# Kernel optimization log

Measured on AMD Instinct MI355X. Metric: run time of the kernel, lower is better.

## Reference

```python
import jax, jax.numpy as jnp
import numpy as np

B, N, E, M, H = 2, 4096, 65536, 4, 256


def setup_inputs() -> dict:
    key = jax.random.key(0)
    ks = jax.random.split(key, 8)
    src = jax.random.randint(ks[0], (B, E), 0, N, dtype=jnp.int32)
    # targets: permutation of arange(E) % N per batch -> every node has >=1 incoming edge
    base = jnp.arange(E, dtype=jnp.int32) % N
    tgt = jnp.stack([jax.random.permutation(jax.random.fold_in(ks[1], b), base) for b in range(B)], axis=0)
    cfg_indices_padded = jnp.stack([src, tgt], axis=-1)  # [B, E, 2]
    hint_state = jax.random.normal(ks[2], (B, N, M, H), dtype=jnp.float32)
    node_fts = jax.random.normal(ks[3], (B, N, M, H), dtype=jnp.float32)
    edge_fts = jax.random.normal(ks[4], (B, E, H), dtype=jnp.float32)
    # hk.Linear default init scales
    edge_W = jax.random.truncated_normal(ks[5], -2.0, 2.0, (H, 1), dtype=jnp.float32) / np.sqrt(H)
    edge_b = jnp.zeros((1,), dtype=jnp.float32)
    update_W = jax.random.truncated_normal(ks[6], -2.0, 2.0, (H, H), dtype=jnp.float32) / np.sqrt(H)
    update_b = jnp.zeros((H,), dtype=jnp.float32)
    return {
        'cfg_indices_padded': cfg_indices_padded,
        'hint_state': hint_state,
        'node_fts': node_fts,
        'edge_fts': edge_fts,
        'edge_W': edge_W,
        'edge_b': edge_b,
        'update_W': update_W,
        'update_b': update_b,
    }


def reference(cfg_indices_padded, hint_state, node_fts, edge_fts, edge_W, edge_b, update_W, update_b):
    nb_nodes = node_fts.shape[1]
    src = cfg_indices_padded[..., 0]  # [B, E]
    tgt = cfg_indices_padded[..., 1]  # [B, E]
    # gather hint states at edge sources: [B, E, M, H]
    hint_sources = jnp.take_along_axis(hint_state, src[:, :, None, None], axis=1)
    # learned per-edge scalar coefficient: [B, E, 1]
    edge_coeff = edge_fts @ edge_W + edge_b
    hint_sources = edge_coeff[..., None] * hint_sources  # [B, E, M, H]
    # segment_max scatter-reduce per batch element -> [B, N, M, H]
    seg_max = jax.vmap(lambda d, s: jax.ops.segment_max(d, s, num_segments=nb_nodes))
    aggregated_hint = seg_max(hint_sources, tgt)
    # final linear update
    return (node_fts + aggregated_hint) @ update_W + update_b
```

## Files before the change

kernel.cpp:

```cpp
#include <hip/hip_runtime.h>

#define BB 2
#define NN 4096
#define EE 65536
#define MM 4
#define HH 256
#define NPB 32
#define NXCD 8
#define XPAD 264

typedef float vf4 __attribute__((ext_vector_type(4)));
typedef int vi2 __attribute__((ext_vector_type(2)));
typedef _Float16 vh4 __attribute__((ext_vector_type(4)));
typedef _Float16 f16x8 __attribute__((ext_vector_type(8)));
typedef float f32x4 __attribute__((ext_vector_type(4)));

#define PREP_A 8192
#define PREP_B 8192
#define PREP_C 64

__global__ __launch_bounds__(256) void k_prep(const float* __restrict__ edge_fts,
                                              const float* __restrict__ edge_W,
                                              const float* __restrict__ edge_b,
                                              const int* __restrict__ cfg,
                                              unsigned int* __restrict__ cnt,
                                              int2* __restrict__ packed,
                                              const float* __restrict__ hint,
                                              _Float16* __restrict__ h16,
                                              const float* __restrict__ W,
                                              _Float16* __restrict__ wt_hi) {
  const int blk = blockIdx.x;
  const int t = threadIdx.x;
  if (blk < PREP_A) {
    const int e0 = blk * 16 + (t >> 6) * 4;
    const int lane = t & 63;
    const float4 wv = *reinterpret_cast<const float4*>(edge_W + lane * 4);
    vf4 ef[4];
#pragma unroll
    for (int q = 0; q < 4; ++q)
      ef[q] = __builtin_nontemporal_load(
          reinterpret_cast<const vf4*>(edge_fts + (size_t)(e0 + q) * HH + lane * 4));
    float s[4];
#pragma unroll
    for (int q = 0; q < 4; ++q)
      s[q] = ef[q].x * wv.x + ef[q].y * wv.y + ef[q].z * wv.z + ef[q].w * wv.w;
#pragma unroll
    for (int off = 32; off > 0; off >>= 1) {
#pragma unroll
      for (int q = 0; q < 4; ++q) s[q] += __shfl_down(s[q], off);
    }
    if (lane == 0) {
      const float eb = edge_b[0];
#pragma unroll
      for (int q = 0; q < 4; ++q) {
        const int widx = e0 + q;
        const int b = widx >> 16;
        const vi2 st = __builtin_nontemporal_load(
            reinterpret_cast<const vi2*>(cfg + (size_t)widx * 2));
        const int slot = b * NN + st.y;
        const unsigned p = atomicAdd(&cnt[slot], 1u) & 15u;
        int2 v;
        v.x = st.x;
        v.y = __float_as_int(s[q] + eb);
        packed[(size_t)slot * 16 + p] = v;
      }
    }
  } else if (blk < PREP_A + PREP_B) {
    const size_t i = (size_t)(blk - PREP_A) * 256 + t;
    const vf4 v = __builtin_nontemporal_load(reinterpret_cast<const vf4*>(hint) + i);
    vh4 h;
    h.x = (_Float16)v.x; h.y = (_Float16)v.y; h.z = (_Float16)v.z; h.w = (_Float16)v.w;
    *(reinterpret_cast<vh4*>(h16) + i) = h;
  } else {
    const int jb = blk - PREP_A - PREP_B;
    const int j = jb * 4 + (t >> 6);
    const int h0 = (t & 63) * 4;
    vh4 hi;
    hi.x = (_Float16)W[(size_t)(h0 + 0) * HH + j];
    hi.y = (_Float16)W[(size_t)(h0 + 1) * HH + j];
    hi.z = (_Float16)W[(size_t)(h0 + 2) * HH + j];
    hi.w = (_Float16)W[(size_t)(h0 + 3) * HH + j];
    *reinterpret_cast<vh4*>(wt_hi + (size_t)j * HH + h0) = hi;
  }
}

__device__ __forceinline__ float4 fmax4(const float4& a, const float4& b) {
  return make_float4(fmaxf(a.x, b.x), fmaxf(a.y, b.y), fmaxf(a.z, b.z), fmaxf(a.w, b.w));
}

__device__ __forceinline__ float4 scmul(float c, const vh4& h) {
  return make_float4(c * (float)h.x, c * (float)h.y, c * (float)h.z, c * (float)h.w);
}

__global__ __launch_bounds__(256, 4) void k_fused(const _Float16* __restrict__ h16,
                                                  const float* __restrict__ node_fts,
                                                  const int2* __restrict__ packed,
                                                  const _Float16* __restrict__ wt_hi,
                                                  const float* __restrict__ bias,
                                                  float* __restrict__ out) {
  __shared__ _Float16 xs_hi[NPB][XPAD];
  __shared__ _Float16 xs_lo[NPB][XPAD];
  __shared__ int ssrc[NPB][16];
  __shared__ float scf[NPB][16];

  const int t = threadIdx.x;
  const int unit = blockIdx.x & (NXCD - 1);
  const int chunk = blockIdx.x >> 3;
  const int b = unit >> 2;
  const int m = unit & 3;
  const int n0 = chunk * NPB;
  const int w = t >> 6;
  const int lane = t & 63;
  const int r0 = w * 8;

#pragma unroll
  for (int q = 0; q < 2; ++q) {
    const int idx = q * 64 + lane;
    const int i = idx >> 4, k = idx & 15;
    const int node = b * NN + n0 + r0 + i;
    const int2 v = packed[(size_t)node * 16 + k];
    ssrc[r0 + i][k] = v.x;
    scf[r0 + i][k] = __int_as_float(v.y);
  }

  const _Float16* hb = h16 + (size_t)b * NN * MM * HH + m * HH + lane * 4;

#pragma unroll 1
  for (int i = 0; i < 8; ++i) {
    const int lr = r0 + i;
    const int n = n0 + lr;
    vh4 hv[16];
#pragma unroll
    for (int k = 0; k < 16; ++k) {
      const int s = ssrc[lr][k];
      hv[k] = *reinterpret_cast<const vh4*>(hb + (size_t)s * (MM * HH));
    }
    float4 t8[8];
#pragma unroll
    for (int k = 0; k < 8; ++k)
      t8[k] = fmax4(scmul(scf[lr][2 * k], hv[2 * k]),
                    scmul(scf[lr][2 * k + 1], hv[2 * k + 1]));
#pragma unroll
    for (int k = 0; k < 4; ++k) t8[k] = fmax4(t8[k], t8[k + 4]);
    t8[0] = fmax4(t8[0], t8[2]);
    t8[1] = fmax4(t8[1], t8[3]);
    const float4 a = fmax4(t8[0], t8[1]);
    const vf4 nf = __builtin_nontemporal_load(reinterpret_cast<const vf4*>(
        node_fts + (((size_t)(b * NN + n) * MM + m) * HH) + lane * 4));
    const float x0 = nf.x + a.x, x1 = nf.y + a.y, x2 = nf.z + a.z, x3 = nf.w + a.w;
    vh4 hi, lo;
    hi.x = (_Float16)x0; lo.x = (_Float16)(x0 - (float)hi.x);
    hi.y = (_Float16)x1; lo.y = (_Float16)(x1 - (float)hi.y);
    hi.z = (_Float16)x2; lo.z = (_Float16)(x2 - (float)hi.z);
    hi.w = (_Float16)x3; lo.w = (_Float16)(x3 - (float)hi.w);
    *reinterpret_cast<vh4*>(&xs_hi[lr][lane * 4]) = hi;
    *reinterpret_cast<vh4*>(&xs_lo[lr][lane * 4]) = lo;
  }
  __syncthreads();

  const int lr16 = lane & 15;
  const int kg = lane >> 4;

#pragma unroll 1
  for (int ct = 0; ct < 4; ++ct) {
    const int j = (w * 4 + ct) * 16 + lr16;
    const _Float16* bh = wt_hi + (size_t)j * HH + kg * 8;
    f16x8 bhi[8];
#pragma unroll
    for (int kt = 0; kt < 8; ++kt)
      bhi[kt] = *reinterpret_cast<const f16x8*>(bh + kt * 32);
    f32x4 acc0 = {0.f, 0.f, 0.f, 0.f};
    f32x4 acc1 = {0.f, 0.f, 0.f, 0.f};
#pragma unroll
    for (int kt = 0; kt < 8; ++kt) {
      const int o = kt * 32 + kg * 8;
      const f16x8 a0h = *reinterpret_cast<const f16x8*>(&xs_hi[lr16][o]);
      const f16x8 a1h = *reinterpret_cast<const f16x8*>(&xs_hi[16 + lr16][o]);
      const f16x8 a0l = *reinterpret_cast<const f16x8*>(&xs_lo[lr16][o]);
      const f16x8 a1l = *reinterpret_cast<const f16x8*>(&xs_lo[16 + lr16][o]);
      acc0 = __builtin_amdgcn_mfma_f32_16x16x32_f16(a0h, bhi[kt], acc0, 0, 0, 0);
      acc1 = __builtin_amdgcn_mfma_f32_16x16x32_f16(a1h, bhi[kt], acc1, 0, 0, 0);
      acc0 = __builtin_amdgcn_mfma_f32_16x16x32_f16(a0l, bhi[kt], acc0, 0, 0, 0);
      acc1 = __builtin_amdgcn_mfma_f32_16x16x32_f16(a1l, bhi[kt], acc1, 0, 0, 0);
    }
    const float bj = bias[j];
#pragma unroll
    for (int r = 0; r < 4; ++r) {
      const int na = n0 + kg * 4 + r;
      const int nb = na + 16;
      __builtin_nontemporal_store(
          acc0[r] + bj, out + (((size_t)(b * NN + na) * MM + m) * HH) + j);
      __builtin_nontemporal_store(
          acc1[r] + bj, out + (((size_t)(b * NN + nb) * MM + m) * HH) + j);
    }
  }
}

extern "C" void kernel_launch(void* const* d_in, const int* in_sizes, int n_in,
                              void* d_out, int out_size, void* d_ws, size_t ws_size,
                              hipStream_t stream) {
  const int* cfg = (const int*)d_in[0];
  const float* hint = (const float*)d_in[1];
  const float* node_fts = (const float*)d_in[2];
  const float* edge_fts = (const float*)d_in[3];
  const float* edge_W = (const float*)d_in[4];
  const float* edge_b = (const float*)d_in[5];
  const float* update_W = (const float*)d_in[6];
  const float* update_b = (const float*)d_in[7];
  float* out = (float*)d_out;

  char* ws = (char*)d_ws;
  unsigned int* cnt = (unsigned int*)ws;
  int2* packed = (int2*)(ws + 32768);
  _Float16* h16 = (_Float16*)(ws + 32768 + 1048576);
  _Float16* wt_hi = (_Float16*)(ws + 32768 + 1048576 + 16777216);

  k_prep<<<PREP_A + PREP_B + PREP_C, 256, 0, stream>>>(
      edge_fts, edge_W, edge_b, cfg, cnt, packed, hint, h16, update_W, wt_hi);
  k_fused<<<BB * MM * (NN / NPB), 256, 0, stream>>>(h16, node_fts, packed,
                                                    wt_hi, update_b, out);
}
```

Baseline: 99.31 us.

## Drop hi/lo split of activations and halve node tile per block

The activation operand of the update GEMM is now stored as a single fp16 value instead of an fp16 hi/lo pair, so half the MFMAs and half the LDS traffic go away. The node tile per block shrinks from 32 to 16 and the occupancy hint rises from 4 to 8 blocks per CU, doubling the grid to add parallelism for the latency-bound gather phase. The B operand is now loaded per k-step instead of being preloaded. The cost is lower precision in the matmul input, which may fail a tight tolerance, and the weight tile is reloaded by twice as many blocks.

```diff
diff --git a/kernel.cpp b/kernel.cpp
--- a/kernel.cpp
+++ b/kernel.cpp
@@ -5,7 +5,7 @@
 #define EE 65536
 #define MM 4
 #define HH 256
-#define NPB 32
+#define NPB 16
 #define NXCD 8
 #define XPAD 264
 
@@ -92,14 +92,13 @@
   return make_float4(c * (float)h.x, c * (float)h.y, c * (float)h.z, c * (float)h.w);
 }
 
-__global__ __launch_bounds__(256, 4) void k_fused(const _Float16* __restrict__ h16,
+__global__ __launch_bounds__(256, 8) void k_fused(const _Float16* __restrict__ h16,
                                                   const float* __restrict__ node_fts,
                                                   const int2* __restrict__ packed,
                                                   const _Float16* __restrict__ wt_hi,
                                                   const float* __restrict__ bias,
                                                   float* __restrict__ out) {
-  __shared__ _Float16 xs_hi[NPB][XPAD];
-  __shared__ _Float16 xs_lo[NPB][XPAD];
+  __shared__ _Float16 xs[NPB][XPAD];
   __shared__ int ssrc[NPB][16];
   __shared__ float scf[NPB][16];
 
@@ -111,22 +110,19 @@
   const int n0 = chunk * NPB;
   const int w = t >> 6;
   const int lane = t & 63;
-  const int r0 = w * 8;
-
-#pragma unroll
-  for (int q = 0; q < 2; ++q) {
-    const int idx = q * 64 + lane;
-    const int i = idx >> 4, k = idx & 15;
-    const int node = b * NN + n0 + r0 + i;
-    const int2 v = packed[(size_t)node * 16 + k];
-    ssrc[r0 + i][k] = v.x;
-    scf[r0 + i][k] = __int_as_float(v.y);
+  const int r0 = w * 4;
+
+  {
+    const int i = t >> 4, k = t & 15;
+    const int2 v = packed[(size_t)(b * NN + n0 + i) * 16 + k];
+    ssrc[i][k] = v.x;
+    scf[i][k] = __int_as_float(v.y);
   }
 
   const _Float16* hb = h16 + (size_t)b * NN * MM * HH + m * HH + lane * 4;
 
 #pragma unroll 1
-  for (int i = 0; i < 8; ++i) {
+  for (int i = 0; i < 4; ++i) {
     const int lr = r0 + i;
     const int n = n0 + lr;
     vh4 hv[16];
@@ -147,14 +143,12 @@
     const float4 a = fmax4(t8[0], t8[1]);
     const vf4 nf = __builtin_nontemporal_load(reinterpret_cast<const vf4*>(
         node_fts + (((size_t)(b * NN + n) * MM + m) * HH) + lane * 4));
-    const float x0 = nf.x + a.x, x1 = nf.y + a.y, x2 = nf.z + a.z, x3 = nf.w + a.w;
-    vh4 hi, lo;
-    hi.x = (_Float16)x0; lo.x = (_Float16)(x0 - (float)hi.x);
-    hi.y = (_Float16)x1; lo.y = (_Float16)(x1 - (float)hi.y);
-    hi.z = (_Float16)x2; lo.z = (_Float16)(x2 - (float)hi.z);
-    hi.w = (_Float16)x3; lo.w = (_Float16)(x3 - (float)hi.w);
-    *reinterpret_cast<vh4*>(&xs_hi[lr][lane * 4]) = hi;
-    *reinterpret_cast<vh4*>(&xs_lo[lr][lane * 4]) = lo;
+    vh4 xq;
+    xq.x = (_Float16)(nf.x + a.x);
+    xq.y = (_Float16)(nf.y + a.y);
+    xq.z = (_Float16)(nf.z + a.z);
+    xq.w = (_Float16)(nf.w + a.w);
+    *reinterpret_cast<vh4*>(&xs[lr][lane * 4]) = xq;
   }
   __syncthreads();
 
@@ -165,33 +159,19 @@
   for (int ct = 0; ct < 4; ++ct) {
     const int j = (w * 4 + ct) * 16 + lr16;
     const _Float16* bh = wt_hi + (size_t)j * HH + kg * 8;
-    f16x8 bhi[8];
-#pragma unroll
-    for (int kt = 0; kt < 8; ++kt)
-      bhi[kt] = *reinterpret_cast<const f16x8*>(bh + kt * 32);
-    f32x4 acc0 = {0.f, 0.f, 0.f, 0.f};
-    f32x4 acc1 = {0.f, 0.f, 0.f, 0.f};
+    f32x4 acc = {0.f, 0.f, 0.f, 0.f};
 #pragma unroll
     for (int kt = 0; kt < 8; ++kt) {
-      const int o = kt * 32 + kg * 8;
-      const f16x8 a0h = *reinterpret_cast<const f16x8*>(&xs_hi[lr16][o]);
-      const f16x8 a1h = *reinterpret_cast<const f16x8*>(&xs_hi[16 + lr16][o]);
-      const f16x8 a0l = *reinterpret_cast<const f16x8*>(&xs_lo[lr16][o]);
-      const f16x8 a1l = *reinterpret_cast<const f16x8*>(&xs_lo[16 + lr16][o]);
-      acc0 = __builtin_amdgcn_mfma_f32_16x16x32_f16(a0h, bhi[kt], acc0, 0, 0, 0);
-      acc1 = __builtin_amdgcn_mfma_f32_16x16x32_f16(a1h, bhi[kt], acc1, 0, 0, 0);
-      acc0 = __builtin_amdgcn_mfma_f32_16x16x32_f16(a0l, bhi[kt], acc0, 0, 0, 0);
-      acc1 = __builtin_amdgcn_mfma_f32_16x16x32_f16(a1l, bhi[kt], acc1, 0, 0, 0);
+      const f16x8 bhi = *reinterpret_cast<const f16x8*>(bh + kt * 32);
+      const f16x8 a = *reinterpret_cast<const f16x8*>(&xs[lr16][kt * 32 + kg * 8]);
+      acc = __builtin_amdgcn_mfma_f32_16x16x32_f16(a, bhi, acc, 0, 0, 0);
     }
     const float bj = bias[j];
 #pragma unroll
     for (int r = 0; r < 4; ++r) {
-      const int na = n0 + kg * 4 + r;
-      const int nb = na + 16;
+      const int n = n0 + kg * 4 + r;
       __builtin_nontemporal_store(
-          acc0[r] + bj, out + (((size_t)(b * NN + na) * MM + m) * HH) + j);
-      __builtin_nontemporal_store(
-          acc1[r] + bj, out + (((size_t)(b * NN + nb) * MM + m) * HH) + j);
+          acc[r] + bj, out + (((size_t)(b * NN + n) * MM + m) * HH) + j);
     }
   }
 }
```

New measurement: 96.68 us. 1.03x faster.
